# Optimization experiments

Measured on AMD Instinct MI355X. Metric: run time of the kernel, lower is better.

Reference implementation:

```python
import jax, jax.numpy as jnp
import numpy as np

P = 2013265921  # BabyBear prime, 15*2^27 + 1 (NTT-friendly stand-in for the 256-bit BLS12-381 field)
GEN = 31        # generator of the multiplicative group of F_P
COSET_G = 3     # coset shift generator
B, N = 8, 1 << 22


def _pow_table(base, n, p):
    """[1, base, base^2, ..., base^{n-1}] mod p via log-doubling (numpy, exact int64)."""
    t = np.ones(n, dtype=np.int64)
    cur = base % p
    k = 1
    while k < n:
        m = min(k, n - k)
        t[k:k + m] = (t[:m] * cur) % p
        cur = (cur * cur) % p
        k *= 2
    return t


def _bitrev(n):
    logn = n.bit_length() - 1
    idx = np.arange(n, dtype=np.int64)
    r = np.zeros(n, dtype=np.int64)
    for i in range(logn):
        r = (r << 1) | ((idx >> i) & 1)
    return r


def _ntt(x, tw, brev, p):
    """Iterative Cooley-Tukey DIT NTT. x: [B, N] int64 in [0, p). tw: [N/2] powers of omega."""
    b, n = x.shape
    x = x[:, brev]
    m = 2
    while m <= n:
        half = m // 2
        w = tw[:: n // m][:half]              # omega^{k * N/m}, k = 0..half-1
        x = x.reshape(b, n // m, m)
        u = x[:, :, :half]
        v = (x[:, :, half:] * w) % p          # < 2^62, safe in int64
        x = jnp.concatenate([(u + v) % p, (u - v) % p], axis=-1).reshape(b, n)
        m *= 2
    return x


def setup_inputs() -> dict:
    key = jax.random.key(0)
    inp = jax.random.randint(key, (B, N), 0, P, dtype=jnp.int64)
    omega = pow(GEN, (P - 1) // N, P)
    omega_inv = pow(omega, -1, P)
    twiddles = jnp.asarray(_pow_table(omega, N // 2, P))
    inv_twiddles = jnp.asarray(_pow_table(omega_inv, N // 2, P))
    coset_powers = jnp.asarray(_pow_table(COSET_G, N, P))
    inv_coset_powers = jnp.asarray(_pow_table(pow(COSET_G, -1, P), N, P))
    bitrev = jnp.asarray(_bitrev(N))
    return {
        "input": inp,
        "twiddles": twiddles,
        "inv_twiddles": inv_twiddles,
        "coset_powers": coset_powers,
        "inv_coset_powers": inv_coset_powers,
        "bitrev": bitrev,
        "is_intt": 0,
        "is_coset": 1,
    }


def reference(input, twiddles, inv_twiddles, coset_powers, inv_coset_powers, bitrev, is_intt, is_coset):
    n = input.shape[-1]
    if is_intt and is_coset:
        out = _ntt(input, inv_twiddles, bitrev, P)
        out = (out * pow(n, -1, P)) % P
        out = (out * inv_coset_powers) % P
    elif is_intt:
        out = _ntt(input, inv_twiddles, bitrev, P)
        out = (out * pow(n, -1, P)) % P
    elif is_coset:
        x = (input * coset_powers) % P
        out = _ntt(x, twiddles, bitrev, P)
    else:
        out = _ntt(input, twiddles, bitrev, P)
    return out
```

## Files before the change

### kernel.cpp

```cpp
#include <hip/hip_runtime.h>
#include <stdint.h>

#define P_MOD       2013265921u
#define TWO32_MOD_P 268435454u

__device__ __forceinline__ uint32_t umin32(uint32_t a, uint32_t b) { return a < b ? a : b; }

__device__ __forceinline__ uint32_t wrapmod(uint32_t z) {
    uint32_t t = z - ((uint32_t)((int32_t)z >> 31) & TWO32_MOD_P);
    return umin32(t, t - P_MOD);
}
__device__ __forceinline__ uint32_t addmod_w(uint32_t u, uint32_t t2) {
    return wrapmod(u + t2);
}
__device__ __forceinline__ uint32_t submod_w(uint32_t u, uint32_t t2) {
    uint32_t d = u - t2;
    return umin32(d, d + P_MOD);
}
__device__ __forceinline__ uint32_t mulmod_wrap(uint32_t a, uint32_t b) {
    return wrapmod(a * b);
}
__device__ __forceinline__ void bf_w(uint32_t& u, uint32_t& v, uint32_t w) {
    uint32_t t  = mulmod_wrap(v, w);
    uint32_t nu = addmod_w(u, t);
    v = submod_w(u, t);
    u = nu;
}

__host__ __device__ constexpr uint32_t compute_pinv_neg() {
    uint32_t x = 1u;
    for (int i = 0; i < 5; ++i) x *= (2u - P_MOD * x);
    return 0u - x;
}
#define PINV_NEG (compute_pinv_neg())
constexpr uint32_t R2_MOD_P = (uint32_t)(((unsigned __int128)1 << 64) % P_MOD);

__device__ __forceinline__ uint32_t montmul(uint32_t a, uint32_t b) {
    uint32_t lo = a * b;
    uint32_t hi = __umulhi(a, b);
    uint32_t m  = lo * PINV_NEG;
    uint32_t t  = hi + __umulhi(m, P_MOD) + (lo != 0u);
    return umin32(t, t - P_MOD);
}

typedef uint32_t u32x4 __attribute__((ext_vector_type(4)));
__device__ __forceinline__ uint4 nt_load4(const uint32_t* p) {
    u32x4 v = __builtin_nontemporal_load(reinterpret_cast<const u32x4*>(p));
    return make_uint4(v.x, v.y, v.z, v.w);
}
__device__ __forceinline__ void nt_store4(uint32_t* p, uint4 x) {
    u32x4 v = {x.x, x.y, x.z, x.w};
    __builtin_nontemporal_store(v, reinterpret_cast<u32x4*>(p));
}

__global__ __launch_bounds__(256) void ntt_pack(
    const uint32_t* __restrict__ tw,
    const uint32_t* __restrict__ itw,
    const int* __restrict__ f_intt,
    uint32_t* __restrict__ ptw, int logn)
{
    int idx = blockIdx.x * 256 + threadIdx.x;
    if (idx >= 8128) return;
    const uint32_t* __restrict__ twsel = f_intt[0] ? itw : tw;
    uint32_t v = (uint32_t)idx + 64u;
    int pm1 = 31 - __clz(v);
    int j   = (int)(v - (1u << pm1));
    int pa  = pm1 + 1;
    ptw[idx] = twsel[(uint32_t)j << (logn - pa)];
}

__global__ __launch_bounds__(256, 4) void ntt_k1(
    const uint32_t* __restrict__ in,
    const uint32_t* __restrict__ tw,
    const uint32_t* __restrict__ itw,
    const uint32_t* __restrict__ cp,
    const int* __restrict__ f_intt,
    const int* __restrict__ f_coset,
    uint32_t* __restrict__ out,
    int logn)
{
    __shared__ uint32_t sh[64 * 65];
    __shared__ uint32_t shT[32];
    const int tid = threadIdx.x;
    const int w   = blockIdx.x;
    const long long base = (long long)blockIdx.y << logn;

    const int is_intt  = f_intt[0];
    const bool do_coset = (!is_intt) && (f_coset[0] != 0);
    const uint32_t* __restrict__ twsel = is_intt ? itw : tw;

    if (tid < 32) shT[tid] = twsel[(uint32_t)tid << (logn - 6)];

    const uint32_t wrev = __brev((uint32_t)w) >> (32 - (logn - 12));

    const int s4 = tid & 15;
    const uint32_t ub = __brev((uint32_t)s4) >> 28;
    for (int it = 0; it < 4; ++it) {
        int c = (it << 4) | (tid >> 4);
        uint32_t crev = __brev((uint32_t)c) >> 26;
        long long src = ((long long)crev << (logn - 6)) |
                        ((long long)wrev << 6) | (unsigned)(s4 << 2);
        uint4 x = nt_load4(in + base + src);
        if (do_coset) {
            uint4 cv = nt_load4(cp + src);
            x.x = mulmod_wrap(x.x, cv.x);
            x.y = mulmod_wrap(x.y, cv.y);
            x.z = mulmod_wrap(x.z, cv.z);
            x.w = mulmod_wrap(x.w, cv.w);
        }
        sh[(ub     ) * 65 + c] = x.x;
        sh[(ub + 32) * 65 + c] = x.y;
        sh[(ub + 16) * 65 + c] = x.z;
        sh[(ub + 48) * 65 + c] = x.w;
    }
    __syncthreads();

#pragma unroll
    for (int pa = 1; pa <= 5; pa += 2) {
        const int hs = 1 << (pa - 1);
        const int row = tid & 63;
        for (int it = 0; it < 4; ++it) {
            int q    = (tid >> 6) + (it << 2);
            int cj   = q & (hs - 1);
            int cblk = q >> (pa - 1);
            int c0   = (cblk << (pa + 1)) | cj;
            int b    = row * 65 + c0;
            uint32_t e0 = sh[b], e1 = sh[b + hs], e2 = sh[b + 2*hs], e3 = sh[b + 3*hs];
            uint32_t w0 = shT[cj << (6 - pa)];
            uint32_t w1 = shT[cj << (5 - pa)];
            uint32_t w2 = shT[(cj + hs) << (5 - pa)];
            bf_w(e0, e1, w0);
            bf_w(e2, e3, w0);
            bf_w(e0, e2, w1);
            bf_w(e1, e3, w2);
            sh[b] = e0; sh[b + hs] = e1; sh[b + 2*hs] = e2; sh[b + 3*hs] = e3;
        }
        __syncthreads();
    }

    for (int it = 0; it < 4; ++it) {
        int u  = (it << 4) | (tid >> 4);
        int cb = (tid & 15) << 2;
        uint4 x;
        x.x = sh[u * 65 + cb    ];
        x.y = sh[u * 65 + cb + 1];
        x.z = sh[u * 65 + cb + 2];
        x.w = sh[u * 65 + cb + 3];
        long long dst = ((long long)u << (logn - 6)) |
                        ((long long)w << 6) | (unsigned)cb;
        *(uint4*)(out + base + dst) = x;
    }
}

__global__ __launch_bounds__(512, 4) void ntt_k2(
    const uint32_t* __restrict__ tw,
    const uint32_t* __restrict__ itw,
    const int* __restrict__ f_intt,
    const uint32_t* __restrict__ ptw,
    uint32_t* __restrict__ data,
    int logn)
{
    alignas(16) __shared__ uint32_t sh[8192];
    const int tid = threadIdx.x;
    const long long base = ((long long)blockIdx.y << logn) +
                           ((long long)blockIdx.x << 13);
    const uint32_t* __restrict__ twsel = f_intt[0] ? itw : tw;

    for (int it = 0; it < 4; ++it) {
        int t4 = tid + it * 512;
        ((uint4*)sh)[t4] = nt_load4(data + base + (t4 << 2));
    }
    __syncthreads();

#pragma unroll
    for (int pa = 7; pa <= 11; pa += 2) {
        const int hs  = 1 << (pa - 1);
        const int pb0 = hs - 64;
        const int pb1 = 2 * hs - 64;
        int q    = tid;
        int jq   = q & ((hs >> 2) - 1);
        int sblk = q >> (pa - 3);
        int j    = jq << 2;
        int i0   = (sblk << (pa + 1)) | j;
        uint4 e0 = *(const uint4*)&sh[i0];
        uint4 e1 = *(const uint4*)&sh[i0 + hs];
        uint4 e2 = *(const uint4*)&sh[i0 + 2*hs];
        uint4 e3 = *(const uint4*)&sh[i0 + 3*hs];
        uint4 w0, w1a, w1b;
        if (ptw) {
            w0  = *(const uint4*)&ptw[pb0 + j];
            w1a = *(const uint4*)&ptw[pb1 + j];
            w1b = *(const uint4*)&ptw[pb1 + hs + j];
        } else {
            const int t0s = logn - pa, t1s = logn - pa - 1;
            w0  = make_uint4(twsel[(uint32_t)(j)<<t0s], twsel[(uint32_t)(j+1)<<t0s],
                             twsel[(uint32_t)(j+2)<<t0s], twsel[(uint32_t)(j+3)<<t0s]);
            w1a = make_uint4(twsel[(uint32_t)(j)<<t1s], twsel[(uint32_t)(j+1)<<t1s],
                             twsel[(uint32_t)(j+2)<<t1s], twsel[(uint32_t)(j+3)<<t1s]);
            w1b = make_uint4(twsel[(uint32_t)(j+hs)<<t1s], twsel[(uint32_t)(j+hs+1)<<t1s],
                             twsel[(uint32_t)(j+hs+2)<<t1s], twsel[(uint32_t)(j+hs+3)<<t1s]);
        }
        bf_w(e0.x, e1.x, w0.x); bf_w(e0.y, e1.y, w0.y);
        bf_w(e0.z, e1.z, w0.z); bf_w(e0.w, e1.w, w0.w);
        bf_w(e2.x, e3.x, w0.x); bf_w(e2.y, e3.y, w0.y);
        bf_w(e2.z, e3.z, w0.z); bf_w(e2.w, e3.w, w0.w);
        bf_w(e0.x, e2.x, w1a.x); bf_w(e0.y, e2.y, w1a.y);
        bf_w(e0.z, e2.z, w1a.z); bf_w(e0.w, e2.w, w1a.w);
        bf_w(e1.x, e3.x, w1b.x); bf_w(e1.y, e3.y, w1b.y);
        bf_w(e1.z, e3.z, w1b.z); bf_w(e1.w, e3.w, w1b.w);
        *(uint4*)&sh[i0         ] = e0;
        *(uint4*)&sh[i0 +   hs  ] = e1;
        *(uint4*)&sh[i0 + 2*hs  ] = e2;
        *(uint4*)&sh[i0 + 3*hs  ] = e3;
        __syncthreads();
    }

    {
        const int hs = 4096, pb = hs - 64;
        for (int it = 0; it < 2; ++it) {
            int j  = (tid + it * 512) << 2;
            uint4 u = *(const uint4*)&sh[j];
            uint4 v = *(const uint4*)&sh[j + hs];
            uint4 wv;
            if (ptw) wv = *(const uint4*)&ptw[pb + j];
            else {
                const int ts = logn - 13;
                wv = make_uint4(twsel[(uint32_t)(j)<<ts], twsel[(uint32_t)(j+1)<<ts],
                                twsel[(uint32_t)(j+2)<<ts], twsel[(uint32_t)(j+3)<<ts]);
            }
            bf_w(u.x, v.x, wv.x); bf_w(u.y, v.y, wv.y);
            bf_w(u.z, v.z, wv.z); bf_w(u.w, v.w, wv.w);
            *(uint4*)&sh[j] = u;
            *(uint4*)&sh[j + hs] = v;
        }
        __syncthreads();
    }

    for (int it = 0; it < 4; ++it) {
        int t4 = tid + it * 512;
        ((uint4*)(data + base))[t4] = ((const uint4*)sh)[t4];
    }
}

__global__ __launch_bounds__(1024, 4) void ntt_k3(
    const uint32_t* __restrict__ tw,
    const uint32_t* __restrict__ itw,
    const uint32_t* __restrict__ icp,
    const int* __restrict__ f_intt,
    const int* __restrict__ f_coset,
    uint32_t* __restrict__ data,
    uint32_t ninv, int logn)
{
    alignas(16) __shared__ uint32_t sh[512 * 32];
    alignas(16) __shared__ uint32_t shB[9 * 32];
    __shared__ uint32_t shA[511];
    const int tid = threadIdx.x;
    const long long base = (long long)blockIdx.y << logn;
    const int lowbase = blockIdx.x * 32;

    const int is_intt  = f_intt[0];
    const int is_coset = f_coset[0];
    const uint32_t* __restrict__ twsel = is_intt ? itw : tw;

    if (tid < 511) {
        uint32_t v = (uint32_t)tid + 1u;
        int p  = 31 - __clz(v);
        int sj = (int)(v - (1u << p));
        shA[tid] = montmul(twsel[(uint32_t)sj << (21 - p)], R2_MOD_P);
    } else if (tid >= 512 && tid < 512 + 288) {
        int k = tid - 512, p = k >> 5, lo = k & 31;
        shB[k] = twsel[(uint32_t)(lowbase + lo) << (8 - p)];
    }

    for (int it = 0; it < 4; ++it) {
        int e4  = tid + it * 1024;
        int lo4 = e4 & 7;
        int s   = e4 >> 3;
        uint4 x = nt_load4(data + base + ((long long)s << 13) + lowbase + (lo4 << 2));
        *(uint4*)&sh[(s << 5) | (lo4 << 2)] = x;
    }
    __syncthreads();

#pragma unroll
    for (int p = 0; p <= 6; p += 3) {
        const int hs = 1 << p;
        for (int it = 0; it < 2; ++it) {
            int wi = tid + it * 1024;
            int lo = wi & 31;
            int sq = wi >> 5;
            int sj = sq & (hs - 1);
            int sblk = sq >> p;
            int s0 = (sblk << (p + 3)) | sj;
            int b  = (s0 << 5) | lo;
            const int st = hs << 5;
            uint32_t e0 = sh[b        ], e1 = sh[b +   st],
                     e2 = sh[b + 2*st], e3 = sh[b + 3*st],
                     e4 = sh[b + 4*st], e5 = sh[b + 5*st],
                     e6 = sh[b + 6*st], e7 = sh[b + 7*st];
            uint32_t b0 = shB[((p    ) << 5) | lo];
            uint32_t b1 = shB[((p + 1) << 5) | lo];
            uint32_t b2 = shB[((p + 2) << 5) | lo];
            uint32_t tw0  = montmul(shA[(    hs - 1) + sj         ], b0);
            uint32_t tw1a = montmul(shA[(2 * hs - 1) + sj         ], b1);
            uint32_t tw1b = montmul(shA[(2 * hs - 1) + sj +     hs], b1);
            uint32_t tw2a = montmul(shA[(4 * hs - 1) + sj         ], b2);
            uint32_t tw2b = montmul(shA[(4 * hs - 1) + sj +     hs], b2);
            uint32_t tw2c = montmul(shA[(4 * hs - 1) + sj + 2 * hs], b2);
            uint32_t tw2d = montmul(shA[(4 * hs - 1) + sj + 3 * hs], b2);
            bf_w(e0, e1, tw0); bf_w(e2, e3, tw0);
            bf_w(e4, e5, tw0); bf_w(e6, e7, tw0);
            bf_w(e0, e2, tw1a); bf_w(e1, e3, tw1b);
            bf_w(e4, e6, tw1a); bf_w(e5, e7, tw1b);
            bf_w(e0, e4, tw2a); bf_w(e1, e5, tw2b);
            bf_w(e2, e6, tw2c); bf_w(e3, e7, tw2d);
            sh[b        ] = e0; sh[b +   st] = e1;
            sh[b + 2*st] = e2; sh[b + 3*st] = e3;
            sh[b + 4*st] = e4; sh[b + 5*st] = e5;
            sh[b + 6*st] = e6; sh[b + 7*st] = e7;
        }
        __syncthreads();
    }

    for (int it = 0; it < 4; ++it) {
        int e4  = tid + it * 1024;
        int lo4 = e4 & 7;
        int s   = e4 >> 3;
        uint4 val = *(const uint4*)&sh[(s << 5) | (lo4 << 2)];
        long long gi = ((long long)s << 13) + lowbase + (lo4 << 2);
        if (is_intt) {
            val.x = mulmod_wrap(val.x, ninv);
            val.y = mulmod_wrap(val.y, ninv);
            val.z = mulmod_wrap(val.z, ninv);
            val.w = mulmod_wrap(val.w, ninv);
            if (is_coset) {
                uint4 ic = *(const uint4*)(icp + gi);
                val.x = mulmod_wrap(val.x, ic.x);
                val.y = mulmod_wrap(val.y, ic.y);
                val.z = mulmod_wrap(val.z, ic.z);
                val.w = mulmod_wrap(val.w, ic.w);
            }
        }
        nt_store4(data + base + gi, val);
    }
}

extern "C" void kernel_launch(void* const* d_in, const int* in_sizes, int n_in,
                              void* d_out, int out_size, void* d_ws, size_t ws_size,
                              hipStream_t stream) {
    const uint32_t* in  = (const uint32_t*)d_in[0];
    const uint32_t* tw  = (const uint32_t*)d_in[1];
    const uint32_t* itw = (const uint32_t*)d_in[2];
    const uint32_t* cp  = (const uint32_t*)d_in[3];
    const uint32_t* icp = (const uint32_t*)d_in[4];
    const int* f_intt  = (const int*)d_in[6];
    const int* f_coset = (const int*)d_in[7];

    const int N = in_sizes[5];
    const int B = in_sizes[0] / N;
    int logn = 0; while ((1 << logn) < N) ++logn;

    const unsigned long long P = 2013265921ull;
    unsigned long long b = (unsigned long long)N % P, e = P - 2, acc = 1;
    while (e) { if (e & 1) acc = acc * b % P; b = b * b % P; e >>= 1; }
    const uint32_t ninv = (uint32_t)acc;

    uint32_t* out = (uint32_t*)d_out;

    uint32_t* ptw = (ws_size >= 8128u * 4u) ? (uint32_t*)d_ws : nullptr;
    if (ptw) ntt_pack<<<dim3(32), dim3(256), 0, stream>>>(tw, itw, f_intt, ptw, logn);

    dim3 g1(N / 4096, B);
    ntt_k1<<<g1, dim3(256), 0, stream>>>(in, tw, itw, cp, f_intt, f_coset, out, logn);

    dim3 g2(N / 8192, B);
    ntt_k2<<<g2, dim3(512), 0, stream>>>(tw, itw, f_intt, ptw, out, logn);

    dim3 g3(8192 / 32, B);
    ntt_k3<<<g3, dim3(1024), 0, stream>>>(tw, itw, icp, f_intt, f_coset, out, ninv, logn);
}
```

Baseline: 472.0 us.

## Factor coset powers on-chip, fold twiddle packing into k1, prefetch k2 twiddles

The coset multiplier is no longer streamed from the full N-length coset_powers table. Each k1 block rebuilds it as the product of a per-column factor and a per-block factor, loaded once into shared memory and combined with Montgomery multiplies. This removes about a third of k1's global reads at the cost of extra integer multiplies. The separate twiddle-packing launch is merged into the tail of k1 block (0,0), and k2 now loads the next stage's twiddles before each barrier so their latency overlaps the butterflies.

```diff
diff --git a/kernel.cpp b/kernel.cpp
--- a/kernel.cpp
+++ b/kernel.cpp
@@ -51,22 +51,6 @@
 __device__ __forceinline__ void nt_store4(uint32_t* p, uint4 x) {
     u32x4 v = {x.x, x.y, x.z, x.w};
     __builtin_nontemporal_store(v, reinterpret_cast<u32x4*>(p));
-}
-
-__global__ __launch_bounds__(256) void ntt_pack(
-    const uint32_t* __restrict__ tw,
-    const uint32_t* __restrict__ itw,
-    const int* __restrict__ f_intt,
-    uint32_t* __restrict__ ptw, int logn)
-{
-    int idx = blockIdx.x * 256 + threadIdx.x;
-    if (idx >= 8128) return;
-    const uint32_t* __restrict__ twsel = f_intt[0] ? itw : tw;
-    uint32_t v = (uint32_t)idx + 64u;
-    int pm1 = 31 - __clz(v);
-    int j   = (int)(v - (1u << pm1));
-    int pa  = pm1 + 1;
-    ptw[idx] = twsel[(uint32_t)j << (logn - pa)];
 }
 
 __global__ __launch_bounds__(256, 4) void ntt_k1(
@@ -77,10 +61,13 @@
     const int* __restrict__ f_intt,
     const int* __restrict__ f_coset,
     uint32_t* __restrict__ out,
+    uint32_t* __restrict__ ptw,
     int logn)
 {
     __shared__ uint32_t sh[64 * 65];
     __shared__ uint32_t shT[32];
+    __shared__ uint32_t shG1[64];
+    alignas(16) __shared__ uint32_t shGW[64];
     const int tid = threadIdx.x;
     const int w   = blockIdx.x;
     const long long base = (long long)blockIdx.y << logn;
@@ -89,9 +76,20 @@
     const bool do_coset = (!is_intt) && (f_coset[0] != 0);
     const uint32_t* __restrict__ twsel = is_intt ? itw : tw;
 
-    if (tid < 32) shT[tid] = twsel[(uint32_t)tid << (logn - 6)];
-
     const uint32_t wrev = __brev((uint32_t)w) >> (32 - (logn - 12));
+
+    if (tid < 32) {
+        shT[tid] = twsel[(uint32_t)tid << (logn - 6)];
+    } else if (tid >= 128 && tid < 192) {
+        int m = tid - 128;
+        uint32_t t1 = cp[(long long)(__brev((uint32_t)m) >> 26) << (logn - 6)];
+        shG1[m] = montmul(t1, R2_MOD_P);
+    } else if (tid >= 192) {
+        int s = tid - 192;
+        uint32_t mgw = montmul(cp[(uint32_t)wrev << 6], R2_MOD_P);
+        shGW[s] = montmul(mgw, cp[s]);
+    }
+    __syncthreads();
 
     const int s4 = tid & 15;
     const uint32_t ub = __brev((uint32_t)s4) >> 28;
@@ -102,11 +100,12 @@
                         ((long long)wrev << 6) | (unsigned)(s4 << 2);
         uint4 x = nt_load4(in + base + src);
         if (do_coset) {
-            uint4 cv = nt_load4(cp + src);
-            x.x = mulmod_wrap(x.x, cv.x);
-            x.y = mulmod_wrap(x.y, cv.y);
-            x.z = mulmod_wrap(x.z, cv.z);
-            x.w = mulmod_wrap(x.w, cv.w);
+            uint32_t mg1 = shG1[c];
+            uint4 g = *(const uint4*)&shGW[s4 << 2];
+            x.x = mulmod_wrap(x.x, montmul(mg1, g.x));
+            x.y = mulmod_wrap(x.y, montmul(mg1, g.y));
+            x.z = mulmod_wrap(x.z, montmul(mg1, g.z));
+            x.w = mulmod_wrap(x.w, montmul(mg1, g.w));
         }
         sh[(ub     ) * 65 + c] = x.x;
         sh[(ub + 32) * 65 + c] = x.y;
@@ -150,6 +149,15 @@
                         ((long long)w << 6) | (unsigned)cb;
         *(uint4*)(out + base + dst) = x;
     }
+
+    if (ptw && blockIdx.x == 0 && blockIdx.y == 0) {
+        for (int i = tid; i < 8128; i += 256) {
+            uint32_t v = (uint32_t)i + 64u;
+            int pm1 = 31 - __clz(v);
+            int j   = (int)(v - (1u << pm1));
+            ptw[i] = twsel[(uint32_t)j << (logn - pm1 - 1)];
+        }
+    }
 }
 
 __global__ __launch_bounds__(512, 4) void ntt_k2(
@@ -166,6 +174,24 @@
                            ((long long)blockIdx.x << 13);
     const uint32_t* __restrict__ twsel = f_intt[0] ? itw : tw;
 
+    uint4 w0, w1a, w1b;
+    {
+        const int j = (tid & 15) << 2;
+        if (ptw) {
+            w0  = *(const uint4*)&ptw[j];
+            w1a = *(const uint4*)&ptw[64 + j];
+            w1b = *(const uint4*)&ptw[128 + j];
+        } else {
+            const int t0s = logn - 7, t1s = logn - 8;
+            w0  = make_uint4(twsel[(uint32_t)(j)<<t0s], twsel[(uint32_t)(j+1)<<t0s],
+                             twsel[(uint32_t)(j+2)<<t0s], twsel[(uint32_t)(j+3)<<t0s]);
+            w1a = make_uint4(twsel[(uint32_t)(j)<<t1s], twsel[(uint32_t)(j+1)<<t1s],
+                             twsel[(uint32_t)(j+2)<<t1s], twsel[(uint32_t)(j+3)<<t1s]);
+            w1b = make_uint4(twsel[(uint32_t)(j+64)<<t1s], twsel[(uint32_t)(j+65)<<t1s],
+                             twsel[(uint32_t)(j+66)<<t1s], twsel[(uint32_t)(j+67)<<t1s]);
+        }
+    }
+
     for (int it = 0; it < 4; ++it) {
         int t4 = tid + it * 512;
         ((uint4*)sh)[t4] = nt_load4(data + base + (t4 << 2));
@@ -174,32 +200,47 @@
 
 #pragma unroll
     for (int pa = 7; pa <= 11; pa += 2) {
-        const int hs  = 1 << (pa - 1);
-        const int pb0 = hs - 64;
-        const int pb1 = 2 * hs - 64;
-        int q    = tid;
-        int jq   = q & ((hs >> 2) - 1);
-        int sblk = q >> (pa - 3);
-        int j    = jq << 2;
-        int i0   = (sblk << (pa + 1)) | j;
+        const int hs = 1 << (pa - 1);
+        uint4 n0, n1a, n1b;
+        if (pa < 11) {
+            const int hsn = hs << 2;
+            const int jn  = (tid & ((hsn >> 2) - 1)) << 2;
+            if (ptw) {
+                n0  = *(const uint4*)&ptw[(hsn - 64) + jn];
+                n1a = *(const uint4*)&ptw[(2*hsn - 64) + jn];
+                n1b = *(const uint4*)&ptw[(2*hsn - 64) + hsn + jn];
+            } else {
+                const int t0s = logn - pa - 2, t1s = logn - pa - 3;
+                n0  = make_uint4(twsel[(uint32_t)(jn)<<t0s], twsel[(uint32_t)(jn+1)<<t0s],
+                                 twsel[(uint32_t)(jn+2)<<t0s], twsel[(uint32_t)(jn+3)<<t0s]);
+                n1a = make_uint4(twsel[(uint32_t)(jn)<<t1s], twsel[(uint32_t)(jn+1)<<t1s],
+                                 twsel[(uint32_t)(jn+2)<<t1s], twsel[(uint32_t)(jn+3)<<t1s]);
+                n1b = make_uint4(twsel[(uint32_t)(jn+hsn)<<t1s], twsel[(uint32_t)(jn+hsn+1)<<t1s],
+                                 twsel[(uint32_t)(jn+hsn+2)<<t1s], twsel[(uint32_t)(jn+hsn+3)<<t1s]);
+            }
+        } else {
+            const int j1 = tid << 2, j2 = (tid + 512) << 2;
+            if (ptw) {
+                n0  = *(const uint4*)&ptw[4032 + j1];
+                n1a = *(const uint4*)&ptw[4032 + j2];
+            } else {
+                const int ts = logn - 13;
+                n0  = make_uint4(twsel[(uint32_t)(j1)<<ts], twsel[(uint32_t)(j1+1)<<ts],
+                                 twsel[(uint32_t)(j1+2)<<ts], twsel[(uint32_t)(j1+3)<<ts]);
+                n1a = make_uint4(twsel[(uint32_t)(j2)<<ts], twsel[(uint32_t)(j2+1)<<ts],
+                                 twsel[(uint32_t)(j2+2)<<ts], twsel[(uint32_t)(j2+3)<<ts]);
+            }
+            n1b = n0;
+        }
+
+        const int jq   = tid & ((hs >> 2) - 1);
+        const int sblk = tid >> (pa - 3);
+        const int j    = jq << 2;
+        const int i0   = (sblk << (pa + 1)) | j;
         uint4 e0 = *(const uint4*)&sh[i0];
         uint4 e1 = *(const uint4*)&sh[i0 + hs];
         uint4 e2 = *(const uint4*)&sh[i0 + 2*hs];
         uint4 e3 = *(const uint4*)&sh[i0 + 3*hs];
-        uint4 w0, w1a, w1b;
-        if (ptw) {
-            w0  = *(const uint4*)&ptw[pb0 + j];
-            w1a = *(const uint4*)&ptw[pb1 + j];
-            w1b = *(const uint4*)&ptw[pb1 + hs + j];
-        } else {
-            const int t0s = logn - pa, t1s = logn - pa - 1;
-            w0  = make_uint4(twsel[(uint32_t)(j)<<t0s], twsel[(uint32_t)(j+1)<<t0s],
-                             twsel[(uint32_t)(j+2)<<t0s], twsel[(uint32_t)(j+3)<<t0s]);
-            w1a = make_uint4(twsel[(uint32_t)(j)<<t1s], twsel[(uint32_t)(j+1)<<t1s],
-                             twsel[(uint32_t)(j+2)<<t1s], twsel[(uint32_t)(j+3)<<t1s]);
-            w1b = make_uint4(twsel[(uint32_t)(j+hs)<<t1s], twsel[(uint32_t)(j+hs+1)<<t1s],
-                             twsel[(uint32_t)(j+hs+2)<<t1s], twsel[(uint32_t)(j+hs+3)<<t1s]);
-        }
         bf_w(e0.x, e1.x, w0.x); bf_w(e0.y, e1.y, w0.y);
         bf_w(e0.z, e1.z, w0.z); bf_w(e0.w, e1.w, w0.w);
         bf_w(e2.x, e3.x, w0.x); bf_w(e2.y, e3.y, w0.y);
@@ -213,28 +254,27 @@
         *(uint4*)&sh[i0 + 2*hs  ] = e2;
         *(uint4*)&sh[i0 + 3*hs  ] = e3;
         __syncthreads();
+        w0 = n0; w1a = n1a; w1b = n1b;
     }
 
     {
-        const int hs = 4096, pb = hs - 64;
-        for (int it = 0; it < 2; ++it) {
-            int j  = (tid + it * 512) << 2;
-            uint4 u = *(const uint4*)&sh[j];
-            uint4 v = *(const uint4*)&sh[j + hs];
-            uint4 wv;
-            if (ptw) wv = *(const uint4*)&ptw[pb + j];
-            else {
-                const int ts = logn - 13;
-                wv = make_uint4(twsel[(uint32_t)(j)<<ts], twsel[(uint32_t)(j+1)<<ts],
-                                twsel[(uint32_t)(j+2)<<ts], twsel[(uint32_t)(j+3)<<ts]);
-            }
-            bf_w(u.x, v.x, wv.x); bf_w(u.y, v.y, wv.y);
-            bf_w(u.z, v.z, wv.z); bf_w(u.w, v.w, wv.w);
-            *(uint4*)&sh[j] = u;
-            *(uint4*)&sh[j + hs] = v;
-        }
-        __syncthreads();
-    }
+        const int hs = 4096;
+        int j = tid << 2;
+        uint4 u = *(const uint4*)&sh[j];
+        uint4 v = *(const uint4*)&sh[j + hs];
+        bf_w(u.x, v.x, w0.x); bf_w(u.y, v.y, w0.y);
+        bf_w(u.z, v.z, w0.z); bf_w(u.w, v.w, w0.w);
+        *(uint4*)&sh[j] = u;
+        *(uint4*)&sh[j + hs] = v;
+        j = (tid + 512) << 2;
+        uint4 u2 = *(const uint4*)&sh[j];
+        uint4 v2 = *(const uint4*)&sh[j + hs];
+        bf_w(u2.x, v2.x, w1a.x); bf_w(u2.y, v2.y, w1a.y);
+        bf_w(u2.z, v2.z, w1a.z); bf_w(u2.w, v2.w, w1a.w);
+        *(uint4*)&sh[j] = u2;
+        *(uint4*)&sh[j + hs] = v2;
+    }
+    __syncthreads();
 
     for (int it = 0; it < 4; ++it) {
         int t4 = tid + it * 512;
@@ -365,12 +405,10 @@
     const uint32_t ninv = (uint32_t)acc;
 
     uint32_t* out = (uint32_t*)d_out;
-
     uint32_t* ptw = (ws_size >= 8128u * 4u) ? (uint32_t*)d_ws : nullptr;
-    if (ptw) ntt_pack<<<dim3(32), dim3(256), 0, stream>>>(tw, itw, f_intt, ptw, logn);
 
     dim3 g1(N / 4096, B);
-    ntt_k1<<<g1, dim3(256), 0, stream>>>(in, tw, itw, cp, f_intt, f_coset, out, logn);
+    ntt_k1<<<g1, dim3(256), 0, stream>>>(in, tw, itw, cp, f_intt, f_coset, out, ptw, logn);
 
     dim3 g2(N / 8192, B);
     ntt_k2<<<g2, dim3(512), 0, stream>>>(tw, itw, f_intt, ptw, out, logn);
```

New measurement: 449.5 us. -4.8%, faster.
